# Optimization experiments

Measured on AMD Instinct MI355X. Metric: run time of the kernel, lower is better.

## Reference

```python
import jax, jax.numpy as jnp
import numpy as np

C = 1024
H = 16
EPS = 1e-5

def layernorm(x, g, b):
    mu = jnp.mean(x, axis=-1, keepdims=True)
    var = jnp.var(x, axis=-1, keepdims=True)
    return (x - mu) * jax.lax.rsqrt(var + EPS) * g + b

def setup_inputs() -> dict:
    key = jax.random.key(0)
    ks = jax.random.split(key, 12)
    s = lambda fan: 1.0 / np.sqrt(fan)
    return {
        "x": jax.random.normal(ks[0], (2, 2048, C), jnp.float32),
        "W_qkv": jax.random.uniform(ks[1], (C, 3 * C), jnp.float32, -s(C), s(C)),
        "W_o": jax.random.uniform(ks[2], (C, C), jnp.float32, -s(C), s(C)),
        "b_o": jnp.zeros((C,), jnp.float32),
        "g1": jnp.ones((C,), jnp.float32),
        "beta1": jnp.zeros((C,), jnp.float32),
        "g2": jnp.ones((C,), jnp.float32),
        "beta2": jnp.zeros((C,), jnp.float32),
        "W_ff1": jax.random.uniform(ks[3], (C, 4 * C), jnp.float32, -s(C), s(C)),
        "b_ff1": jnp.zeros((4 * C,), jnp.float32),
        "W_ff2": jax.random.uniform(ks[4], (4 * C, C), jnp.float32, -s(4 * C), s(4 * C)),
        "b_ff2": jnp.zeros((C,), jnp.float32),
    }

def reference(x, W_qkv, W_o, b_o, g1, beta1, g2, beta2, W_ff1, b_ff1, W_ff2, b_ff2):
    B, T, _ = x.shape
    hd = C // H  # head dim
    # --- self-attention on norm1(x) ---
    h = layernorm(x, g1, beta1)
    qkv = h @ W_qkv                      # [B,T,3C]
    q, k, v = jnp.split(qkv, 3, axis=-1)
    reshp = lambda t: t.reshape(B, T, H, hd).transpose(0, 2, 1, 3)  # [B,H,T,hd]
    q, k, v = reshp(q), reshp(k), reshp(v)
    att = jnp.einsum("bhqd,bhkd->bhqk", q, k) * (hd ** -0.5)
    causal = jnp.tril(jnp.ones((T, T), bool))
    att = jnp.where(causal, att, -jnp.inf)
    att = jax.nn.softmax(att, axis=-1)
    out = jnp.einsum("bhqk,bhkd->bhqd", att, v)
    out = out.transpose(0, 2, 1, 3).reshape(B, T, C)
    x = x + out @ W_o + b_o
    # --- feed-forward on norm2(x) ---
    h = layernorm(x, g2, beta2)
    h = jax.nn.relu(h @ W_ff1 + b_ff1) @ W_ff2 + b_ff2
    return x + h
```

## Files before the change

### kernel.cpp

```cpp
#include <hip/hip_runtime.h>
#include <hip/hip_bf16.h>
#include <stdint.h>


typedef __attribute__((ext_vector_type(8))) short bf16x8;
typedef __attribute__((ext_vector_type(4))) float f32x4;

#define MFMA16(a, b, c) __builtin_amdgcn_mfma_f32_16x16x32_bf16((a), (b), (c), 0, 0, 0)

__device__ __forceinline__ void gload16(const void* g, void* l) {
    __builtin_amdgcn_global_load_lds(
        (const __attribute__((address_space(1))) char*)g,
        (__attribute__((address_space(3))) char*)l, 16, 0, 0);
}

__device__ __forceinline__ int xcd_swizzle(int flat, int nblk) {
    if ((nblk & 7) == 0) {
        const int per = nblk >> 3;
        flat = (flat & 7) * per + (flat >> 3);
    }
    return flat;
}

__global__ __launch_bounds__(256) void tconv_all(
    const float* __restrict__ w0, __hip_bfloat16* __restrict__ o0,
    const float* __restrict__ w1, __hip_bfloat16* __restrict__ o1,
    const float* __restrict__ w2, __hip_bfloat16* __restrict__ o2,
    const float* __restrict__ w3, __hip_bfloat16* __restrict__ o3) {
    __shared__ float tile[64][33];
    const int f = blockIdx.x;
    const float* in; __hip_bfloat16* out; int K, N, nx, t;
    if (f < 1536)      { in = w0; out = o0; K = 1024; N = 3072; nx = 96;  t = f; }
    else if (f < 2048) { in = w1; out = o1; K = 1024; N = 1024; nx = 32;  t = f - 1536; }
    else if (f < 4096) { in = w2; out = o2; K = 1024; N = 4096; nx = 128; t = f - 2048; }
    else               { in = w3; out = o3; K = 4096; N = 1024; nx = 32;  t = f - 4096; }
    const int n0 = (t % nx) * 32, k0 = (t / nx) * 64;
    const int tx = threadIdx.x, ty = threadIdx.y;
#pragma unroll
    for (int i = 0; i < 8; i++)
        tile[i * 8 + ty][tx] = in[(size_t)(k0 + i * 8 + ty) * N + n0 + tx];
    __syncthreads();
    for (int i = ty; i < 32; i += 8) {
        const unsigned short lo =
            __bfloat16_as_ushort(__float2bfloat16(tile[2 * tx][i]));
        const unsigned short hi =
            __bfloat16_as_ushort(__float2bfloat16(tile[2 * tx + 1][i]));
        *(uint32_t*)(out + (size_t)(n0 + i) * K + k0 + 2 * tx) =
            ((uint32_t)hi << 16) | lo;
    }
}

__global__ __launch_bounds__(256) void ln_k(const float* __restrict__ x,
                                            const float* __restrict__ g,
                                            const float* __restrict__ beta,
                                            __hip_bfloat16* __restrict__ out) {
    const int row = blockIdx.x;
    const int tid = threadIdx.x;
    float4 v = ((const float4*)(x + (size_t)row * 1024))[tid];
    float s  = v.x + v.y + v.z + v.w;
    float s2 = v.x * v.x + v.y * v.y + v.z * v.z + v.w * v.w;
    for (int off = 1; off < 64; off <<= 1) {
        s  += __shfl_xor(s,  off, 64);
        s2 += __shfl_xor(s2, off, 64);
    }
    __shared__ float ss[4], ss2[4];
    const int w = tid >> 6, lane = tid & 63;
    if (lane == 0) { ss[w] = s; ss2[w] = s2; }
    __syncthreads();
    s  = ss[0] + ss[1] + ss[2] + ss[3];
    s2 = ss2[0] + ss2[1] + ss2[2] + ss2[3];
    const float mu  = s * (1.0f / 1024.0f);
    const float var = s2 * (1.0f / 1024.0f) - mu * mu;
    const float rs  = rsqrtf(var + 1e-5f);
    float4 gv = ((const float4*)g)[tid];
    float4 bv = ((const float4*)beta)[tid];
    __hip_bfloat16* o = out + (size_t)row * 1024 + tid * 4;
    o[0] = __float2bfloat16((v.x - mu) * rs * gv.x + bv.x);
    o[1] = __float2bfloat16((v.y - mu) * rs * gv.y + bv.y);
    o[2] = __float2bfloat16((v.z - mu) * rs * gv.z + bv.z);
    o[3] = __float2bfloat16((v.w - mu) * rs * gv.w + bv.w);
}

template <int BIAS, int RELU, int RESID, int OUTBF>
__global__ __launch_bounds__(256, 2) void gemm_k(const __hip_bfloat16* __restrict__ A,
                                                 const __hip_bfloat16* __restrict__ Bt,
                                                 const float* __restrict__ bias,
                                                 const float* __restrict__ resid,
                                                 void* __restrict__ out,
                                                 int M, int N, int K) {
    __align__(16) __shared__ __hip_bfloat16 As[2][128 * 64];
    __align__(16) __shared__ __hip_bfloat16 Bs[2][128 * 64];

    const int tid  = threadIdx.x;
    const int lane = tid & 63, w = tid >> 6;
    const int wm = w >> 1, wn = w & 1;
    const int nbx = gridDim.x;
    const int flat = xcd_swizzle(blockIdx.y * nbx + blockIdx.x, nbx * gridDim.y);
    const int m0 = (flat / nbx) * 128, n0 = (flat % nbx) * 128;
    const int l16 = lane & 15, quad = lane >> 4;

    const int srw = lane >> 3;
    const int scn = ((lane & 7) - srw) & 7;

    const __hip_bfloat16* ga[4];
    const __hip_bfloat16* gb[4];
#pragma unroll
    for (int i = 0; i < 4; i++) {
        const int row = i * 32 + w * 8 + srw;
        ga[i] = A  + (size_t)(m0 + row) * K + scn * 8;
        gb[i] = Bt + (size_t)(n0 + row) * K + scn * 8;
    }

    int offA[2][4], offB[2][4];
#pragma unroll
    for (int s = 0; s < 2; s++)
#pragma unroll
        for (int t = 0; t < 4; t++) {
            const int rA = wm * 64 + t * 16 + l16;
            offA[s][t] = (rA * 8 + ((s * 4 + quad + (rA & 7)) & 7)) * 16;
            const int rB = wn * 64 + t * 16 + l16;
            offB[s][t] = (rB * 8 + ((s * 4 + quad + (rB & 7)) & 7)) * 16;
        }

    f32x4 acc[4][4] = {};

#pragma unroll
    for (int i = 0; i < 4; i++) {
        gload16(ga[i], As[0] + (i * 256 + w * 64) * 8);
        gload16(gb[i], Bs[0] + (i * 256 + w * 64) * 8);
        ga[i] += 64; gb[i] += 64;
    }

    const int niter = K >> 6;
    for (int it = 0; it < niter; it++) {
        const int buf = it & 1;
        __syncthreads();
        if (it + 1 < niter) {
#pragma unroll
            for (int i = 0; i < 4; i++) {
                gload16(ga[i], As[buf ^ 1] + (i * 256 + w * 64) * 8);
                gload16(gb[i], Bs[buf ^ 1] + (i * 256 + w * 64) * 8);
                ga[i] += 64; gb[i] += 64;
            }
        }

#pragma unroll
        for (int s = 0; s < 2; s++) {
            bf16x8 af[4], bfr[4];
#pragma unroll
            for (int t = 0; t < 4; t++) {
                af[t]  = *(const bf16x8*)((const char*)As[buf] + offA[s][t]);
                bfr[t] = *(const bf16x8*)((const char*)Bs[buf] + offB[s][t]);
            }
#pragma unroll
            for (int mt = 0; mt < 4; mt++)
#pragma unroll
                for (int nt = 0; nt < 4; nt++)
                    acc[mt][nt] = MFMA16(af[mt], bfr[nt], acc[mt][nt]);
        }
    }

#pragma unroll
    for (int mt = 0; mt < 4; mt++)
#pragma unroll
        for (int nt = 0; nt < 4; nt++) {
            const int row = m0 + wm * 64 + mt * 16 + quad * 4;
            const int col = n0 + wn * 64 + nt * 16 + l16;
            const float bv = BIAS ? bias[col] : 0.0f;
#pragma unroll
            for (int r = 0; r < 4; r++) {
                float v = acc[mt][nt][r] + bv;
                if (RELU) v = v > 0.0f ? v : 0.0f;
                const size_t idx = (size_t)(row + r) * N + col;
                if (RESID) v += resid[idx];
                if (OUTBF) ((__hip_bfloat16*)out)[idx] = __float2bfloat16(v);
                else       ((float*)out)[idx] = v;
            }
        }
}

template <int BIAS, int RELU, int RESID, int OUTBF>
__global__ __launch_bounds__(256, 4) void gemm6464_k(const __hip_bfloat16* __restrict__ A,
                                                     const __hip_bfloat16* __restrict__ Bt,
                                                     const float* __restrict__ bias,
                                                     const float* __restrict__ resid,
                                                     void* __restrict__ out,
                                                     int M, int N, int K) {
    __align__(16) __shared__ __hip_bfloat16 As[2][64 * 64];
    __align__(16) __shared__ __hip_bfloat16 Bs[2][64 * 64];

    const int tid  = threadIdx.x;
    const int lane = tid & 63, w = tid >> 6;
    const int wm = w >> 1, wn = w & 1;
    const int nbx = gridDim.x;
    const int flat = xcd_swizzle(blockIdx.y * nbx + blockIdx.x, nbx * gridDim.y);
    const int m0 = (flat / nbx) * 64, n0 = (flat % nbx) * 64;
    const int l16 = lane & 15, quad = lane >> 4;

    const int srw = lane >> 3;
    const int scn = ((lane & 7) - srw) & 7;

    const __hip_bfloat16* ga[2];
    const __hip_bfloat16* gb[2];
#pragma unroll
    for (int i = 0; i < 2; i++) {
        const int row = i * 32 + w * 8 + srw;
        ga[i] = A  + (size_t)(m0 + row) * K + scn * 8;
        gb[i] = Bt + (size_t)(n0 + row) * K + scn * 8;
    }

    int offA[2][2], offB[2][2];
#pragma unroll
    for (int s = 0; s < 2; s++)
#pragma unroll
        for (int t = 0; t < 2; t++) {
            const int rA = wm * 32 + t * 16 + l16;
            offA[s][t] = (rA * 8 + ((s * 4 + quad + (rA & 7)) & 7)) * 16;
            const int rB = wn * 32 + t * 16 + l16;
            offB[s][t] = (rB * 8 + ((s * 4 + quad + (rB & 7)) & 7)) * 16;
        }

    f32x4 acc[2][2] = {};

#pragma unroll
    for (int i = 0; i < 2; i++) {
        gload16(ga[i], As[0] + (i * 256 + w * 64) * 8);
        gload16(gb[i], Bs[0] + (i * 256 + w * 64) * 8);
        ga[i] += 64; gb[i] += 64;
    }

    const int niter = K >> 6;
    for (int it = 0; it < niter; it++) {
        const int buf = it & 1;
        __syncthreads();
        if (it + 1 < niter) {
#pragma unroll
            for (int i = 0; i < 2; i++) {
                gload16(ga[i], As[buf ^ 1] + (i * 256 + w * 64) * 8);
                gload16(gb[i], Bs[buf ^ 1] + (i * 256 + w * 64) * 8);
                ga[i] += 64; gb[i] += 64;
            }
        }

#pragma unroll
        for (int s = 0; s < 2; s++) {
            bf16x8 af[2], bfr[2];
#pragma unroll
            for (int t = 0; t < 2; t++) {
                af[t]  = *(const bf16x8*)((const char*)As[buf] + offA[s][t]);
                bfr[t] = *(const bf16x8*)((const char*)Bs[buf] + offB[s][t]);
            }
#pragma unroll
            for (int mt = 0; mt < 2; mt++)
#pragma unroll
                for (int nt = 0; nt < 2; nt++)
                    acc[mt][nt] = MFMA16(af[mt], bfr[nt], acc[mt][nt]);
        }
    }

#pragma unroll
    for (int mt = 0; mt < 2; mt++)
#pragma unroll
        for (int nt = 0; nt < 2; nt++) {
            const int row = m0 + wm * 32 + mt * 16 + quad * 4;
            const int col = n0 + wn * 32 + nt * 16 + l16;
            const float bv = BIAS ? bias[col] : 0.0f;
#pragma unroll
            for (int r = 0; r < 4; r++) {
                float v = acc[mt][nt][r] + bv;
                if (RELU) v = v > 0.0f ? v : 0.0f;
                const size_t idx = (size_t)(row + r) * N + col;
                if (RESID) v += resid[idx];
                if (OUTBF) ((__hip_bfloat16*)out)[idx] = __float2bfloat16(v);
                else       ((float*)out)[idx] = v;
            }
        }
}

__global__ __launch_bounds__(256) void vtrans_k(const __hip_bfloat16* __restrict__ qkv,
                                                __hip_bfloat16* __restrict__ vt) {
    const int T = 2048, C3 = 3072;
    const int bh = blockIdx.y, b = bh >> 4, h = bh & 15;
    const int t0 = blockIdx.x * 64;
    const int tx = threadIdx.x, ty = threadIdx.y;
    __shared__ __hip_bfloat16 tile[64][65];
#pragma unroll
    for (int j = 0; j < 16; j++) {
        const int tl = ty * 16 + j;
        tile[tl][tx] = qkv[(size_t)(b * T + t0 + tl) * C3 + 2048 + h * 64 + tx];
    }
    __syncthreads();
#pragma unroll
    for (int j = 0; j < 16; j++) {
        const int d = ty * 16 + j;
        vt[((size_t)bh * 64 + d) * 2048 + t0 + tx] = tile[tx][d];
    }
}

__global__ __launch_bounds__(256, 3) void attn_k(const __hip_bfloat16* __restrict__ qkv,
                                                 const __hip_bfloat16* __restrict__ vt,
                                                 __hip_bfloat16* __restrict__ outp) {
    const int T = 2048, C3 = 3072;
    const int bh = blockIdx.x, b = bh >> 4, h = bh & 15;
    const int qt = 31 - blockIdx.y;
    const int q0 = qt * 64;
    const int tid = threadIdx.x, lane = tid & 63, w = tid >> 6;
    const int l16 = lane & 15, quad = lane >> 4;

    __align__(16) __shared__ __hip_bfloat16 Ks[2][64 * 64];
    __align__(16) __shared__ __hip_bfloat16 Vs[2][64 * 64];
    __align__(16) __shared__ __hip_bfloat16 Pw[4][16 * 72];

    const float sc = 0.125f * 1.44269504f;
    bf16x8 qf0, qf1;
    {
        const __hip_bfloat16* qp =
            qkv + (size_t)(b * T + q0 + w * 16 + l16) * C3 + h * 64;
        bf16x8 a = *(const bf16x8*)(qp + quad * 8);
        bf16x8 c = *(const bf16x8*)(qp + 32 + quad * 8);
#pragma unroll
        for (int i = 0; i < 8; i++) {
            union { unsigned int u; float f; } ua, uc;
            ua.u = ((unsigned int)(unsigned short)a[i]) << 16;
            uc.u = ((unsigned int)(unsigned short)c[i]) << 16;
            qf0[i] = (short)(__bfloat16_as_ushort(__float2bfloat16(ua.f * sc)));
            qf1[i] = (short)(__bfloat16_as_ushort(__float2bfloat16(uc.f * sc)));
        }
    }

    const int srw = lane >> 3;
    const int scn = ((lane & 7) - srw) & 7;
    const __hip_bfloat16* kp[2];
    const __hip_bfloat16* vp[2];
#pragma unroll
    for (int i = 0; i < 2; i++) {
        const int row = i * 32 + w * 8 + srw;
        kp[i] = qkv + (size_t)(b * T + row) * C3 + 1024 + h * 64 + scn * 8;
        vp[i] = vt + ((size_t)bh * 64 + row) * 2048 + scn * 8;
    }

    int offK[2][4];
#pragma unroll
    for (int s = 0; s < 2; s++)
#pragma unroll
        for (int t = 0; t < 4; t++) {
            const int rr = t * 16 + l16;
            offK[s][t] = (rr * 8 + ((s * 4 + quad + (rr & 7)) & 7)) * 16;
        }

    f32x4 oacc[4] = {};
    float lpart[4] = {0.0f, 0.0f, 0.0f, 0.0f};

#pragma unroll
    for (int i = 0; i < 2; i++) {
        gload16(kp[i], Ks[0] + (i * 256 + w * 64) * 8);
        gload16(vp[i], Vs[0] + (i * 256 + w * 64) * 8);
    }

    for (int kt = 0; kt <= qt; kt++) {
        const int buf = kt & 1;
        __syncthreads();
        if (kt < qt) {
#pragma unroll
            for (int i = 0; i < 2; i++) {
                gload16(kp[i] + (size_t)(kt + 1) * 64 * C3,
                        Ks[buf ^ 1] + (i * 256 + w * 64) * 8);
                gload16(vp[i] + (kt + 1) * 64,
                        Vs[buf ^ 1] + (i * 256 + w * 64) * 8);
            }
        }

        f32x4 s4[4];
#pragma unroll
        for (int nt = 0; nt < 4; nt++) {
            bf16x8 kf0 = *(const bf16x8*)((const char*)Ks[buf] + offK[0][nt]);
            bf16x8 kf1 = *(const bf16x8*)((const char*)Ks[buf] + offK[1][nt]);
            f32x4 z = {};
            z = MFMA16(qf0, kf0, z);
            z = MFMA16(qf1, kf1, z);
            s4[nt] = z;
        }

        const bool diag = (kt == qt);
        const int myrow = w * 16 + quad * 4;
#pragma unroll
        for (int nt = 0; nt < 4; nt++) {
            const int col = nt * 16 + l16;
#pragma unroll
            for (int r = 0; r < 4; r++) {
                float p = exp2f(s4[nt][r]);
                if (diag && col > myrow + r) p = 0.0f;
                lpart[r] += p;
                Pw[w][(quad * 4 + r) * 72 + col] = __float2bfloat16(p);
            }
        }

        asm volatile("s_waitcnt lgkmcnt(0)" ::: "memory");

        bf16x8 pf0 = *(const bf16x8*)(&Pw[w][l16 * 72 + quad * 8]);
        bf16x8 pf1 = *(const bf16x8*)(&Pw[w][l16 * 72 + 32 + quad * 8]);
#pragma unroll
        for (int dt = 0; dt < 4; dt++) {
            bf16x8 vf0 = *(const bf16x8*)((const char*)Vs[buf] + offK[0][dt]);
            bf16x8 vf1 = *(const bf16x8*)((const char*)Vs[buf] + offK[1][dt]);
            oacc[dt] = MFMA16(pf0, vf0, oacc[dt]);
            oacc[dt] = MFMA16(pf1, vf1, oacc[dt]);
        }
    }

#pragma unroll
    for (int off = 1; off < 16; off <<= 1)
#pragma unroll
        for (int r = 0; r < 4; r++)
            lpart[r] += __shfl_xor(lpart[r], off, 64);

    float rl[4];
#pragma unroll
    for (int r = 0; r < 4; r++) rl[r] = 1.0f / lpart[r];
#pragma unroll
    for (int dt = 0; dt < 4; dt++)
#pragma unroll
        for (int r = 0; r < 4; r++) {
            const int row = q0 + w * 16 + quad * 4 + r;
            outp[(size_t)(b * T + row) * 1024 + h * 64 + dt * 16 + l16] =
                __float2bfloat16(oacc[dt][r] * rl[r]);
        }
}

extern "C" void kernel_launch(void* const* d_in, const int* in_sizes, int n_in,
                              void* d_out, int out_size, void* d_ws, size_t ws_size,
                              hipStream_t stream) {
    const float* x     = (const float*)d_in[0];
    const float* Wqkv  = (const float*)d_in[1];
    const float* Wo    = (const float*)d_in[2];
    const float* b_o   = (const float*)d_in[3];
    const float* g1    = (const float*)d_in[4];
    const float* beta1 = (const float*)d_in[5];
    const float* g2    = (const float*)d_in[6];
    const float* beta2 = (const float*)d_in[7];
    const float* Wff1  = (const float*)d_in[8];
    const float* bff1  = (const float*)d_in[9];
    const float* Wff2  = (const float*)d_in[10];
    const float* bff2  = (const float*)d_in[11];

    char* ws = (char*)d_ws;
    size_t off = 0;
    auto alloc = [&](size_t bytes) {
        void* p = ws + off;
        off += (bytes + 255) & ~(size_t)255;
        return p;
    };
    __hip_bfloat16* Wqkv_t = (__hip_bfloat16*)alloc(3072ULL * 1024 * 2);
    __hip_bfloat16* Wo_t   = (__hip_bfloat16*)alloc(1024ULL * 1024 * 2);
    __hip_bfloat16* Wff1_t = (__hip_bfloat16*)alloc(4096ULL * 1024 * 2);
    __hip_bfloat16* Wff2_t = (__hip_bfloat16*)alloc(1024ULL * 4096 * 2);
    __hip_bfloat16* h_bf   = (__hip_bfloat16*)alloc(4096ULL * 1024 * 2);
    __hip_bfloat16* qkv_bf = (__hip_bfloat16*)alloc(4096ULL * 3072 * 2);
    __hip_bfloat16* att_bf = (__hip_bfloat16*)alloc(4096ULL * 1024 * 2);
    float*          x2     = (float*)alloc(4096ULL * 1024 * 4);
    __hip_bfloat16* ff1_bf = qkv_bf;
    __hip_bfloat16* vt     = (__hip_bfloat16*)x2;

    tconv_all<<<6144, dim3(32, 8), 0, stream>>>(Wqkv, Wqkv_t, Wo, Wo_t,
                                                Wff1, Wff1_t, Wff2, Wff2_t);

    ln_k<<<4096, 256, 0, stream>>>(x, g1, beta1, h_bf);
    gemm_k<0, 0, 0, 1><<<dim3(3072 / 128, 4096 / 128), 256, 0, stream>>>(
        h_bf, Wqkv_t, nullptr, nullptr, qkv_bf, 4096, 3072, 1024);
    vtrans_k<<<dim3(32, 32), dim3(64, 4), 0, stream>>>(qkv_bf, vt);
    attn_k<<<dim3(32, 32), 256, 0, stream>>>(qkv_bf, vt, att_bf);
    gemm6464_k<1, 0, 1, 0><<<dim3(1024 / 64, 4096 / 64), 256, 0, stream>>>(
        att_bf, Wo_t, b_o, x, x2, 4096, 1024, 1024);
    ln_k<<<4096, 256, 0, stream>>>(x2, g2, beta2, h_bf);
    gemm_k<1, 1, 0, 1><<<dim3(4096 / 128, 4096 / 128), 256, 0, stream>>>(
        h_bf, Wff1_t, bff1, nullptr, ff1_bf, 4096, 4096, 1024);
    gemm6464_k<1, 0, 1, 0><<<dim3(1024 / 64, 4096 / 64), 256, 0, stream>>>(
        ff1_bf, Wff2_t, bff2, x2, (float*)d_out, 4096, 1024, 4096);
}
```

Before: 315.1 us.

## Replace 128x128 GEMM with 256x256 eight-wave ping-pong pipelined GEMM

Swaps the 128x128 tile, 4-wave GEMM used for the QKV and FF1 projections for a 256x256 tile, 8-wave kernel. Loads are staged in half-tiles across eight phases per two K-steps, with explicit barriers, vmcnt waits and s_setprio around the MFMA bursts. The aim is more data reuse per tile and better overlap of global-to-LDS loads with matrix math. In exchange it uses 128KB of LDS per block, and the grids become small: 192 blocks for QKV and 256 for FF1, which can leave CUs idle.

```diff
diff --git a/kernel.cpp b/kernel.cpp
--- a/kernel.cpp
+++ b/kernel.cpp
@@ -81,100 +81,140 @@
     o[3] = __float2bfloat16((v.w - mu) * rs * gv.w + bv.w);
 }
 
-template <int BIAS, int RELU, int RESID, int OUTBF>
-__global__ __launch_bounds__(256, 2) void gemm_k(const __hip_bfloat16* __restrict__ A,
-                                                 const __hip_bfloat16* __restrict__ Bt,
-                                                 const float* __restrict__ bias,
-                                                 const float* __restrict__ resid,
-                                                 void* __restrict__ out,
-                                                 int M, int N, int K) {
-    __align__(16) __shared__ __hip_bfloat16 As[2][128 * 64];
-    __align__(16) __shared__ __hip_bfloat16 Bs[2][128 * 64];
+template <int BIAS, int RELU>
+__global__ __launch_bounds__(512, 2) void gemm256_k(const __hip_bfloat16* __restrict__ A,
+                                                    const __hip_bfloat16* __restrict__ Bt,
+                                                    const float* __restrict__ bias,
+                                                    __hip_bfloat16* __restrict__ out,
+                                                    int M, int N, int K) {
+    __align__(16) __shared__ __hip_bfloat16 As[2][2][128 * 64];
+    __align__(16) __shared__ __hip_bfloat16 Bs[2][2][128 * 64];
 
     const int tid  = threadIdx.x;
     const int lane = tid & 63, w = tid >> 6;
-    const int wm = w >> 1, wn = w & 1;
+    const int wm = w >> 2, wn = w & 3;
     const int nbx = gridDim.x;
     const int flat = xcd_swizzle(blockIdx.y * nbx + blockIdx.x, nbx * gridDim.y);
-    const int m0 = (flat / nbx) * 128, n0 = (flat % nbx) * 128;
+    const int m0 = (flat / nbx) * 256, n0 = (flat % nbx) * 256;
     const int l16 = lane & 15, quad = lane >> 4;
 
     const int srw = lane >> 3;
     const int scn = ((lane & 7) - srw) & 7;
 
-    const __hip_bfloat16* ga[4];
-    const __hip_bfloat16* gb[4];
-#pragma unroll
-    for (int i = 0; i < 4; i++) {
-        const int row = i * 32 + w * 8 + srw;
-        ga[i] = A  + (size_t)(m0 + row) * K + scn * 8;
-        gb[i] = Bt + (size_t)(n0 + row) * K + scn * 8;
-    }
-
-    int offA[2][4], offB[2][4];
-#pragma unroll
-    for (int s = 0; s < 2; s++)
+    const __hip_bfloat16* gA[2][2];
+    const __hip_bfloat16* gB[2][2];
+#pragma unroll
+    for (int h = 0; h < 2; h++)
+#pragma unroll
+        for (int i = 0; i < 2; i++) {
+            const int r = h * 128 + i * 64 + w * 8 + srw;
+            gA[h][i] = A  + (size_t)(m0 + r) * K + scn * 8;
+            gB[h][i] = Bt + (size_t)(n0 + r) * K + scn * 8;
+        }
+
+    int offA[2][4], offB[2][2];
+#pragma unroll
+    for (int s = 0; s < 2; s++) {
 #pragma unroll
         for (int t = 0; t < 4; t++) {
-            const int rA = wm * 64 + t * 16 + l16;
-            offA[s][t] = (rA * 8 + ((s * 4 + quad + (rA & 7)) & 7)) * 16;
-            const int rB = wn * 64 + t * 16 + l16;
-            offB[s][t] = (rB * 8 + ((s * 4 + quad + (rB & 7)) & 7)) * 16;
-        }
-
-    f32x4 acc[4][4] = {};
-
-#pragma unroll
-    for (int i = 0; i < 4; i++) {
-        gload16(ga[i], As[0] + (i * 256 + w * 64) * 8);
-        gload16(gb[i], Bs[0] + (i * 256 + w * 64) * 8);
-        ga[i] += 64; gb[i] += 64;
-    }
-
-    const int niter = K >> 6;
-    for (int it = 0; it < niter; it++) {
-        const int buf = it & 1;
-        __syncthreads();
-        if (it + 1 < niter) {
-#pragma unroll
-            for (int i = 0; i < 4; i++) {
-                gload16(ga[i], As[buf ^ 1] + (i * 256 + w * 64) * 8);
-                gload16(gb[i], Bs[buf ^ 1] + (i * 256 + w * 64) * 8);
-                ga[i] += 64; gb[i] += 64;
-            }
-        }
-
-#pragma unroll
-        for (int s = 0; s < 2; s++) {
-            bf16x8 af[4], bfr[4];
-#pragma unroll
-            for (int t = 0; t < 4; t++) {
-                af[t]  = *(const bf16x8*)((const char*)As[buf] + offA[s][t]);
-                bfr[t] = *(const bf16x8*)((const char*)Bs[buf] + offB[s][t]);
-            }
-#pragma unroll
-            for (int mt = 0; mt < 4; mt++)
-#pragma unroll
-                for (int nt = 0; nt < 4; nt++)
-                    acc[mt][nt] = MFMA16(af[mt], bfr[nt], acc[mt][nt]);
-        }
-    }
-
-#pragma unroll
-    for (int mt = 0; mt < 4; mt++)
+            const int r = t * 16 + l16;
+            offA[s][t] = (r * 8 + ((s * 4 + quad + (r & 7)) & 7)) * 16;
+        }
+#pragma unroll
+        for (int t = 0; t < 2; t++) {
+            const int r = (wn & 1) * 64 + t * 16 + l16;
+            offB[s][t] = (r * 8 + ((s * 4 + quad + (r & 7)) & 7)) * 16;
+        }
+    }
+    const char* AsW = (const char*)&As[0][wm][0];
+    const char* BsW = (const char*)&Bs[0][wn >> 1][0];
+
+    f32x4 acc[8][4] = {};
+    bf16x8 a[2][4], b[2][2];
+
+    const int NT = K >> 6;
+
+#define STG_A(ST, SH, D)                                                      \
+    do { if ((ST) < NT) {                                                     \
+        _Pragma("unroll") for (int i = 0; i < 2; i++)                         \
+            gload16(gA[SH][i] + (size_t)(ST) * 64,                            \
+                    &As[D][SH][(i * 64 + w * 8) * 64]);                       \
+    } } while (0)
+#define STG_B(ST, SH, D)                                                      \
+    do { if ((ST) < NT) {                                                     \
+        _Pragma("unroll") for (int i = 0; i < 2; i++)                         \
+            gload16(gB[SH][i] + (size_t)(ST) * 64,                            \
+                    &Bs[D][SH][(i * 64 + w * 8) * 64]);                       \
+    } } while (0)
+#define VM_NONE do {} while (0)
+#define VM_P(X)                                                               \
+    do { if ((X) < NT) asm volatile("s_waitcnt vmcnt(2)" ::: "memory");       \
+         else          asm volatile("s_waitcnt vmcnt(0)" ::: "memory");       \
+    } while (0)
+
+#define PH(RDA, MH, RDB, NH, D, STG, VM)                                      \
+    do {                                                                      \
+        if (RDA) {                                                            \
+            _Pragma("unroll") for (int s = 0; s < 2; s++)                     \
+            _Pragma("unroll") for (int t = 0; t < 4; t++)                     \
+                a[s][t] = *(const bf16x8*)(AsW + (D) * 32768 + (MH) * 8192 +  \
+                                           offA[s][t]);                       \
+        }                                                                     \
+        if (RDB) {                                                            \
+            _Pragma("unroll") for (int s = 0; s < 2; s++)                     \
+            _Pragma("unroll") for (int t = 0; t < 2; t++)                     \
+                b[s][t] = *(const bf16x8*)(BsW + (D) * 32768 + (NH) * 4096 +  \
+                                           offB[s][t]);                       \
+        }                                                                     \
+        STG;                                                                  \
+        __builtin_amdgcn_s_barrier();                                         \
+        asm volatile("" ::: "memory");                                        \
+        __builtin_amdgcn_s_setprio(1);                                        \
+        _Pragma("unroll") for (int s = 0; s < 2; s++)                         \
+        _Pragma("unroll") for (int ti = 0; ti < 4; ti++)                      \
+        _Pragma("unroll") for (int tj = 0; tj < 2; tj++)                      \
+            acc[(MH) * 4 + ti][(NH) * 2 + tj] =                               \
+                MFMA16(a[s][ti], b[s][tj], acc[(MH) * 4 + ti][(NH) * 2 + tj]);\
+        __builtin_amdgcn_s_setprio(0);                                        \
+        VM;                                                                   \
+        __builtin_amdgcn_s_barrier();                                         \
+        asm volatile("" ::: "memory");                                        \
+    } while (0)
+
+    STG_A(0, 0, 0); STG_A(0, 1, 0); STG_B(0, 0, 0); STG_B(0, 1, 0);
+    STG_A(1, 0, 1);
+    asm volatile("s_waitcnt vmcnt(2)" ::: "memory");
+    __builtin_amdgcn_s_barrier();
+    asm volatile("" ::: "memory");
+
+    for (int T = 0; T < NT; T += 2) {
+        PH(1, 0, 1, 0, 0, STG_A(T + 1, 1, 1), VM_NONE);
+        PH(0, 0, 1, 1, 0, STG_B(T + 1, 0, 1), VM_NONE);
+        PH(1, 1, 0, 1, 0, STG_B(T + 1, 1, 1), VM_NONE);
+        PH(0, 1, 1, 0, 0, STG_A(T + 2, 0, 0), VM_P(T + 2));
+        PH(1, 0, 1, 0, 1, STG_A(T + 2, 1, 0), VM_NONE);
+        PH(0, 0, 1, 1, 1, STG_B(T + 2, 0, 0), VM_NONE);
+        PH(1, 1, 0, 1, 1, STG_B(T + 2, 1, 0), VM_NONE);
+        PH(0, 1, 1, 0, 1, STG_A(T + 3, 0, 1), VM_P(T + 3));
+    }
+#undef PH
+#undef VM_P
+#undef VM_NONE
+#undef STG_B
+#undef STG_A
+
+#pragma unroll
+    for (int mt = 0; mt < 8; mt++)
 #pragma unroll
         for (int nt = 0; nt < 4; nt++) {
-            const int row = m0 + wm * 64 + mt * 16 + quad * 4;
+            const int row = m0 + wm * 128 + mt * 16 + quad * 4;
             const int col = n0 + wn * 64 + nt * 16 + l16;
             const float bv = BIAS ? bias[col] : 0.0f;
 #pragma unroll
             for (int r = 0; r < 4; r++) {
                 float v = acc[mt][nt][r] + bv;
                 if (RELU) v = v > 0.0f ? v : 0.0f;
-                const size_t idx = (size_t)(row + r) * N + col;
-                if (RESID) v += resid[idx];
-                if (OUTBF) ((__hip_bfloat16*)out)[idx] = __float2bfloat16(v);
-                else       ((float*)out)[idx] = v;
+                out[(size_t)(row + r) * N + col] = __float2bfloat16(v);
             }
         }
 }
@@ -465,15 +505,15 @@
                                                 Wff1, Wff1_t, Wff2, Wff2_t);
 
     ln_k<<<4096, 256, 0, stream>>>(x, g1, beta1, h_bf);
-    gemm_k<0, 0, 0, 1><<<dim3(3072 / 128, 4096 / 128), 256, 0, stream>>>(
-        h_bf, Wqkv_t, nullptr, nullptr, qkv_bf, 4096, 3072, 1024);
+    gemm256_k<0, 0><<<dim3(3072 / 256, 4096 / 256), 512, 0, stream>>>(
+        h_bf, Wqkv_t, nullptr, qkv_bf, 4096, 3072, 1024);
     vtrans_k<<<dim3(32, 32), dim3(64, 4), 0, stream>>>(qkv_bf, vt);
     attn_k<<<dim3(32, 32), 256, 0, stream>>>(qkv_bf, vt, att_bf);
     gemm6464_k<1, 0, 1, 0><<<dim3(1024 / 64, 4096 / 64), 256, 0, stream>>>(
         att_bf, Wo_t, b_o, x, x2, 4096, 1024, 1024);
     ln_k<<<4096, 256, 0, stream>>>(x2, g2, beta2, h_bf);
-    gemm_k<1, 1, 0, 1><<<dim3(4096 / 128, 4096 / 128), 256, 0, stream>>>(
-        h_bf, Wff1_t, bff1, nullptr, ff1_bf, 4096, 4096, 1024);
+    gemm256_k<1, 1><<<dim3(4096 / 256, 4096 / 256), 512, 0, stream>>>(
+        h_bf, Wff1_t, bff1, ff1_bf, 4096, 4096, 1024);
     gemm6464_k<1, 0, 1, 0><<<dim3(1024 / 64, 4096 / 64), 256, 0, stream>>>(
         ff1_bf, Wff2_t, bff2, x2, (float*)d_out, 4096, 1024, 4096);
 }
```

Result: faster. 307.8 us (-2.3%).
